# Optimization experiments

Measured on AMD Instinct MI355X. Metric: run time of the kernel, lower is better.

## Reference

```python
import jax, jax.numpy as jnp
import numpy as np

NEG_INF = -1e9
T = 0.07

def _l2norm(x, axis):
    return x / jnp.maximum(jnp.linalg.norm(x, axis=axis, keepdims=True), 1e-12)

def setup_inputs() -> dict:
    key = jax.random.key(0)
    ks = jax.random.split(key, 8)
    B, D, K, C = 1024, 128, 131072, 10
    q = jax.random.normal(ks[0], (B, D), dtype=jnp.float32)
    k = jax.random.normal(ks[1], (B, D), dtype=jnp.float32)
    labels = jax.random.randint(ks[2], (B,), 0, C)
    predictions = jax.random.randint(ks[3], (B,), 0, C)
    pos_queue = _l2norm(jax.random.normal(ks[4], (D, K), dtype=jnp.float32), axis=0)
    neg_queue = _l2norm(jax.random.normal(ks[5], (D, K), dtype=jnp.float32), axis=0)
    queue_labels = jax.random.randint(ks[6], (K,), 0, C)
    queue_predictions = jax.random.randint(ks[7], (K,), 0, C)
    return {"q": q, "k": k, "labels": labels, "predictions": predictions,
            "pos_queue": pos_queue, "neg_queue": neg_queue,
            "queue_labels": queue_labels, "queue_predictions": queue_predictions}

def _masked_mean_sim(qn, queue, sel_mask):
    # qn: [B,D], queue: [D,K], sel_mask: [B,K] bool
    sims = jnp.einsum('bd,dk->bk', qn, queue)            # [B,K]
    cnt = sel_mask.sum(axis=1)                           # [B]
    s = jnp.where(sel_mask, sims, 0.0).sum(axis=1)       # [B]
    return jnp.where(cnt > 0, s / jnp.maximum(cnt, 1).astype(sims.dtype), NEG_INF)

def reference(q, k, labels, predictions, pos_queue, neg_queue, queue_labels, queue_predictions):
    qn = _l2norm(q, axis=1)
    _ = _l2norm(k, axis=1)  # k normalized in original forward but unused downstream
    match = queue_predictions[None, :] == predictions[:, None]   # [B,K]
    correct = (queue_predictions == queue_labels)[None, :]       # [1,K]
    pos_mask = match & correct
    neg_mask = match & ~correct
    pos_logits = _masked_mean_sim(qn, pos_queue, pos_mask)       # [B]
    neg_logits = _masked_mean_sim(qn, neg_queue, neg_mask)       # [B]
    logits = jnp.stack([pos_logits, neg_logits], axis=1) / T     # [B,2]
    # cross entropy with target class 0, reduction='none'
    contrast_loss = -jax.nn.log_softmax(logits, axis=1)[:, 0]
    pred = jnp.argmax(logits, axis=1)
    acc = (pred == 0).astype(jnp.float32).mean()
    return contrast_loss, acc
```

## Files before the change

kernel.cpp:

```cpp
#include <hip/hip_runtime.h>

#define K_Q   131072
#define B_N   1024
#define D_DIM 128
#define NCLS  10
#define NC2   (2 * NCLS)
#define CHUNKS 16
#define NEG_INF_F (-1e9f)

__global__ void k_init(int* cnt, int* accCnt) {
    int t = threadIdx.x;
    if (t < NC2) cnt[t] = 0;
    if (t == 0) *accCnt = 0;
}

__global__ void k_code(const int* __restrict__ qp, const int* __restrict__ ql,
                       unsigned char* __restrict__ code, int* __restrict__ cnt) {
    __shared__ int lc[NC2];
    int t = threadIdx.x;
    if (t < NC2) lc[t] = 0;
    __syncthreads();
    int idx = blockIdx.x * blockDim.x + t;
    int stride = gridDim.x * blockDim.x;
    for (int k = idx; k < K_Q; k += stride) {
        int p = qp[k];
        int cd = (p == ql[k]) ? p : (p + NCLS);
        code[k] = (unsigned char)cd;
        atomicAdd(&lc[cd], 1);
    }
    __syncthreads();
    if (t < NC2) atomicAdd(&cnt[t], lc[t]);
}

__global__ __launch_bounds__(256, 4)
void k_reduce(const float* __restrict__ posq, const float* __restrict__ negq,
              const unsigned char* __restrict__ code,
              float* __restrict__ partial) {
    __shared__ float acc[256 * NC2];
    const int d  = blockIdx.y;
    const int ch = blockIdx.x;
    const int t  = threadIdx.x;
    const int span = K_Q / CHUNKS;
    const int k0 = ch * span;

    float* my = &acc[t * NC2];
#pragma unroll
    for (int j = 0; j < NC2; ++j) my[j] = 0.0f;
    __syncthreads();

    const float4* prow = (const float4*)(posq + (size_t)d * K_Q + k0);
    const float4* nrow = (const float4*)(negq + (size_t)d * K_Q + k0);
    const uchar4* crow = (const uchar4*)(code + k0);

    const int iters = span / 4 / 256;

    float4 pv = prow[t];
    float4 nv = nrow[t];
    uchar4 cd = crow[t];

    for (int it = 0; it < iters; ++it) {
        float4 cpv = pv, cnv = nv;
        uchar4 ccd = cd;
        int nx = (it + 1) * 256 + t;
        if (it + 1 < iters) {
            pv = prow[nx];
            nv = nrow[nx];
            cd = crow[nx];
        }
        {
            int c0 = ccd.x; my[c0] += (c0 < NCLS) ? cpv.x : cnv.x;
            int c1 = ccd.y; my[c1] += (c1 < NCLS) ? cpv.y : cnv.y;
            int c2 = ccd.z; my[c2] += (c2 < NCLS) ? cpv.z : cnv.z;
            int c3 = ccd.w; my[c3] += (c3 < NCLS) ? cpv.w : cnv.w;
        }
    }
    __syncthreads();

    if (t < 128) {
#pragma unroll
        for (int j = 0; j < NC2; ++j) acc[t * NC2 + j] += acc[(t + 128) * NC2 + j];
    }
    __syncthreads();
    if (t < 64) {
#pragma unroll
        for (int j = 0; j < NC2; ++j) acc[t * NC2 + j] += acc[(t + 64) * NC2 + j];
    }
    __syncthreads();

    if (t < 64) {
        float r[NC2];
#pragma unroll
        for (int j = 0; j < NC2; ++j) {
            float x = acc[t * NC2 + j];
#pragma unroll
            for (int off = 32; off; off >>= 1) x += __shfl_xor(x, off);
            r[j] = x;
        }
        if (t == 0) {
#pragma unroll
            for (int j = 0; j < NC2; ++j)
                partial[((size_t)d * CHUNKS + ch) * NC2 + j] = r[j];
        }
    }
}

__global__ void k_finalize(const float* __restrict__ partial, float* __restrict__ S) {
    int t = blockIdx.x * blockDim.x + threadIdx.x;
    if (t >= D_DIM * NC2) return;
    int d = t / NC2;
    int j = t % NC2;
    float s = 0.0f;
#pragma unroll
    for (int ch = 0; ch < CHUNKS; ++ch)
        s += partial[((size_t)d * CHUNKS + ch) * NC2 + j];
    S[j * D_DIM + d] = s;
}

__global__ void k_loss(const float* __restrict__ q, const int* __restrict__ preds,
                       const float* __restrict__ S, const int* __restrict__ cnt,
                       float* __restrict__ out, int* __restrict__ accCnt) {
    const int b = blockIdx.x;
    const int t = threadIdx.x;
    const int c = preds[b];

    float qv = q[(size_t)b * D_DIM + t];
    float sp = S[c * D_DIM + t];
    float sn = S[(NCLS + c) * D_DIM + t];
    float s0 = qv * qv, s1 = qv * sp, s2 = qv * sn;

#pragma unroll
    for (int off = 32; off; off >>= 1) {
        s0 += __shfl_xor(s0, off);
        s1 += __shfl_xor(s1, off);
        s2 += __shfl_xor(s2, off);
    }
    __shared__ float red[2][3];
    int wave = t >> 6;
    if ((t & 63) == 0) { red[wave][0] = s0; red[wave][1] = s1; red[wave][2] = s2; }
    __syncthreads();
    if (t == 0) {
        float nq  = red[0][0] + red[1][0];
        float dp  = red[0][1] + red[1][1];
        float dn  = red[0][2] + red[1][2];
        float inv = 1.0f / fmaxf(sqrtf(nq), 1e-12f);
        int cp = cnt[c], cn = cnt[NCLS + c];
        float pl = (cp > 0) ? (dp * inv) / (float)(cp > 1 ? cp : 1) : NEG_INF_F;
        float nl = (cn > 0) ? (dn * inv) / (float)(cn > 1 ? cn : 1) : NEG_INF_F;
        float a  = pl / 0.07f;
        float bb = nl / 0.07f;
        float m  = fmaxf(a, bb);
        float loss = m + logf(expf(a - m) + expf(bb - m)) - a;
        out[b] = loss;
        if (a >= bb) atomicAdd(accCnt, 1);
    }
}

__global__ void k_acc(const int* __restrict__ accCnt, float* __restrict__ out) {
    out[B_N] = (float)(*accCnt) * (1.0f / (float)B_N);
}

extern "C" void kernel_launch(void* const* d_in, const int* in_sizes, int n_in,
                              void* d_out, int out_size, void* d_ws, size_t ws_size,
                              hipStream_t stream) {
    const float* q      = (const float*)d_in[0];
    const int* preds    = (const int*)d_in[3];
    const float* posq   = (const float*)d_in[4];
    const float* negq   = (const float*)d_in[5];
    const int* qlabels  = (const int*)d_in[6];
    const int* qpreds   = (const int*)d_in[7];
    float* out = (float*)d_out;

    char* ws = (char*)d_ws;
    unsigned char* code = (unsigned char*)ws;
    int* cnt            = (int*)(ws + 131072);
    int* accCnt         = (int*)(ws + 131072 + 80);
    float* partial      = (float*)(ws + 131168);
    float* S            = (float*)(ws + 131168 + D_DIM * CHUNKS * NC2 * 4);

    k_init<<<1, 64, 0, stream>>>(cnt, accCnt);
    k_code<<<256, 256, 0, stream>>>(qpreds, qlabels, code, cnt);
    k_reduce<<<dim3(CHUNKS, D_DIM), 256, 0, stream>>>(posq, negq, code, partial);
    k_finalize<<<10, 256, 0, stream>>>(partial, S);
    k_loss<<<B_N, 128, 0, stream>>>(q, preds, S, cnt, out, accCnt);
    k_acc<<<1, 1, 0, stream>>>(accCnt, out);
}
```

Before: 47.62 us.

## Replace scalar class-bucketed reduction with bf16 MFMA one-hot matmul

The per-class sum over the queue is rewritten as a matrix product between one-hot class-indicator matrices and the queue rows, computed with bf16 16x16x32 MFMA instructions. Queue values are converted from fp32 to bf16 in registers, and each block covers a contiguous K slice across all D, writing per-block partials. A two-stage finalize then reduces those partials. This removes the LDS scatter-accumulate, but it adds bf16 rounding error and reads the K dimension through strided per-lane row accesses.

```diff
diff --git a/kernel.cpp b/kernel.cpp
--- a/kernel.cpp
+++ b/kernel.cpp
@@ -1,12 +1,25 @@
 #include <hip/hip_runtime.h>
+#include <hip/hip_bf16.h>
 
 #define K_Q   131072
 #define B_N   1024
 #define D_DIM 128
 #define NCLS  10
-#define NC2   (2 * NCLS)
-#define CHUNKS 16
+#define NC2   20
 #define NEG_INF_F (-1e9f)
+
+#define MBLK  512
+#define MW    4
+#define MSL   2
+#define FCH   8
+
+typedef __attribute__((ext_vector_type(8))) short short8v;
+typedef __attribute__((ext_vector_type(4))) float vf4;
+
+__device__ __forceinline__ short f2bf(float f) {
+    __hip_bfloat16 h = __float2bfloat16(f);
+    return *reinterpret_cast<short*>(&h);
+}
 
 __global__ void k_init(int* cnt, int* accCnt) {
     int t = threadIdx.x;
@@ -32,88 +45,100 @@
     if (t < NC2) atomicAdd(&cnt[t], lc[t]);
 }
 
-__global__ __launch_bounds__(256, 4)
-void k_reduce(const float* __restrict__ posq, const float* __restrict__ negq,
-              const unsigned char* __restrict__ code,
-              float* __restrict__ partial) {
-    __shared__ float acc[256 * NC2];
-    const int d  = blockIdx.y;
-    const int ch = blockIdx.x;
-    const int t  = threadIdx.x;
-    const int span = K_Q / CHUNKS;
-    const int k0 = ch * span;
-
-    float* my = &acc[t * NC2];
-#pragma unroll
-    for (int j = 0; j < NC2; ++j) my[j] = 0.0f;
-    __syncthreads();
-
-    const float4* prow = (const float4*)(posq + (size_t)d * K_Q + k0);
-    const float4* nrow = (const float4*)(negq + (size_t)d * K_Q + k0);
-    const uchar4* crow = (const uchar4*)(code + k0);
-
-    const int iters = span / 4 / 256;
-
-    float4 pv = prow[t];
-    float4 nv = nrow[t];
-    uchar4 cd = crow[t];
-
-    for (int it = 0; it < iters; ++it) {
-        float4 cpv = pv, cnv = nv;
-        uchar4 ccd = cd;
-        int nx = (it + 1) * 256 + t;
-        if (it + 1 < iters) {
-            pv = prow[nx];
-            nv = nrow[nx];
-            cd = crow[nx];
+__global__ __launch_bounds__(256)
+void k_mfma(const float* __restrict__ posq, const float* __restrict__ negq,
+            const unsigned char* __restrict__ code, float* __restrict__ partial) {
+    const int t    = threadIdx.x;
+    const int wave = t >> 6;
+    const int lane = t & 63;
+    const int bid  = blockIdx.x;
+    const int cl   = lane & 15;
+    const int g    = lane >> 4;
+
+    vf4 accp[8], accn[8];
+#pragma unroll
+    for (int i = 0; i < 8; ++i) {
+        accp[i] = (vf4){0.f, 0.f, 0.f, 0.f};
+        accn[i] = (vf4){0.f, 0.f, 0.f, 0.f};
+    }
+
+    for (int s = 0; s < MSL; ++s) {
+        const int gslice = (bid * MW + wave) * MSL + s;
+        const int kl = gslice * 32 + g * 8;
+
+        uint2 cw = *(const uint2*)(code + kl);
+        short8v ap, an;
+#pragma unroll
+        for (int j = 0; j < 8; ++j) {
+            unsigned b = (((j < 4) ? cw.x : cw.y) >> (8 * (j & 3))) & 0xffu;
+            ap[j] = (b == (unsigned)cl)          ? (short)0x3F80 : (short)0;
+            an[j] = (b == (unsigned)(cl + NCLS)) ? (short)0x3F80 : (short)0;
         }
-        {
-            int c0 = ccd.x; my[c0] += (c0 < NCLS) ? cpv.x : cnv.x;
-            int c1 = ccd.y; my[c1] += (c1 < NCLS) ? cpv.y : cnv.y;
-            int c2 = ccd.z; my[c2] += (c2 < NCLS) ? cpv.z : cnv.z;
-            int c3 = ccd.w; my[c3] += (c3 < NCLS) ? cpv.w : cnv.w;
+
+#pragma unroll
+        for (int db = 0; db < 8; ++db) {
+            const int d = db * 16 + cl;
+            const float* pp = posq + (size_t)d * K_Q + kl;
+            const float* np = negq + (size_t)d * K_Q + kl;
+            float4 p0 = ((const float4*)pp)[0];
+            float4 p1 = ((const float4*)pp)[1];
+            float4 n0 = ((const float4*)np)[0];
+            float4 n1 = ((const float4*)np)[1];
+            short8v bp, bn;
+            bp[0] = f2bf(p0.x); bp[1] = f2bf(p0.y); bp[2] = f2bf(p0.z); bp[3] = f2bf(p0.w);
+            bp[4] = f2bf(p1.x); bp[5] = f2bf(p1.y); bp[6] = f2bf(p1.z); bp[7] = f2bf(p1.w);
+            bn[0] = f2bf(n0.x); bn[1] = f2bf(n0.y); bn[2] = f2bf(n0.z); bn[3] = f2bf(n0.w);
+            bn[4] = f2bf(n1.x); bn[5] = f2bf(n1.y); bn[6] = f2bf(n1.z); bn[7] = f2bf(n1.w);
+            accp[db] = __builtin_amdgcn_mfma_f32_16x16x32_bf16(ap, bp, accp[db], 0, 0, 0);
+            accn[db] = __builtin_amdgcn_mfma_f32_16x16x32_bf16(an, bn, accn[db], 0, 0, 0);
         }
     }
-    __syncthreads();
-
-    if (t < 128) {
-#pragma unroll
-        for (int j = 0; j < NC2; ++j) acc[t * NC2 + j] += acc[(t + 128) * NC2 + j];
-    }
-    __syncthreads();
-    if (t < 64) {
-#pragma unroll
-        for (int j = 0; j < NC2; ++j) acc[t * NC2 + j] += acc[(t + 64) * NC2 + j];
-    }
-    __syncthreads();
-
-    if (t < 64) {
-        float r[NC2];
-#pragma unroll
-        for (int j = 0; j < NC2; ++j) {
-            float x = acc[t * NC2 + j];
-#pragma unroll
-            for (int off = 32; off; off >>= 1) x += __shfl_xor(x, off);
-            r[j] = x;
+
+    __shared__ float red[MW][64][8];
+#pragma unroll
+    for (int db = 0; db < 8; ++db) {
+        *(vf4*)&red[wave][lane][0] = accp[db];
+        *(vf4*)&red[wave][lane][4] = accn[db];
+        __syncthreads();
+        if (wave == 0) {
+#pragma unroll
+            for (int r = 0; r < 4; ++r) {
+                int cls = g * 4 + r;
+                if (cls < NCLS) {
+                    float sp = red[0][lane][r]     + red[1][lane][r]
+                             + red[2][lane][r]     + red[3][lane][r];
+                    float sn = red[0][lane][4 + r] + red[1][lane][4 + r]
+                             + red[2][lane][4 + r] + red[3][lane][4 + r];
+                    partial[((size_t)bid * NC2 + cls)        * D_DIM + db * 16 + cl] = sp;
+                    partial[((size_t)bid * NC2 + NCLS + cls) * D_DIM + db * 16 + cl] = sn;
+                }
+            }
         }
-        if (t == 0) {
-#pragma unroll
-            for (int j = 0; j < NC2; ++j)
-                partial[((size_t)d * CHUNKS + ch) * NC2 + j] = r[j];
-        }
-    }
-}
-
-__global__ void k_finalize(const float* __restrict__ partial, float* __restrict__ S) {
-    int t = blockIdx.x * blockDim.x + threadIdx.x;
-    if (t >= D_DIM * NC2) return;
-    int d = t / NC2;
-    int j = t % NC2;
+        __syncthreads();
+    }
+}
+
+__global__ void k_fin1(const float* __restrict__ partial, float* __restrict__ ws2) {
+    int idx = blockIdx.x * blockDim.x + threadIdx.x;
+    if (idx >= FCH * NC2 * D_DIM) return;
+    int chunk = idx / (NC2 * D_DIM);
+    int jd    = idx % (NC2 * D_DIM);
     float s = 0.0f;
-#pragma unroll
-    for (int ch = 0; ch < CHUNKS; ++ch)
-        s += partial[((size_t)d * CHUNKS + ch) * NC2 + j];
-    S[j * D_DIM + d] = s;
+    int b0 = chunk * (MBLK / FCH);
+#pragma unroll 8
+    for (int b = b0; b < b0 + MBLK / FCH; ++b)
+        s += partial[(size_t)b * (NC2 * D_DIM) + jd];
+    ws2[(size_t)chunk * (NC2 * D_DIM) + jd] = s;
+}
+
+__global__ void k_fin2(const float* __restrict__ ws2, float* __restrict__ S) {
+    int jd = blockIdx.x * blockDim.x + threadIdx.x;
+    if (jd >= NC2 * D_DIM) return;
+    float s = 0.0f;
+#pragma unroll
+    for (int ch = 0; ch < FCH; ++ch)
+        s += ws2[(size_t)ch * (NC2 * D_DIM) + jd];
+    S[jd] = s;
 }
 
 __global__ void k_loss(const float* __restrict__ q, const int* __restrict__ preds,
@@ -174,13 +199,15 @@
     unsigned char* code = (unsigned char*)ws;
     int* cnt            = (int*)(ws + 131072);
     int* accCnt         = (int*)(ws + 131072 + 80);
-    float* partial      = (float*)(ws + 131168);
-    float* S            = (float*)(ws + 131168 + D_DIM * CHUNKS * NC2 * 4);
+    float* partial      = (float*)(ws + 131328);
+    float* ws2          = (float*)(ws + 131328 + (size_t)MBLK * NC2 * D_DIM * 4);
+    float* S            = (float*)(ws + 131328 + (size_t)(MBLK + FCH) * NC2 * D_DIM * 4);
 
     k_init<<<1, 64, 0, stream>>>(cnt, accCnt);
     k_code<<<256, 256, 0, stream>>>(qpreds, qlabels, code, cnt);
-    k_reduce<<<dim3(CHUNKS, D_DIM), 256, 0, stream>>>(posq, negq, code, partial);
-    k_finalize<<<10, 256, 0, stream>>>(partial, S);
+    k_mfma<<<MBLK, 256, 0, stream>>>(posq, negq, code, partial);
+    k_fin1<<<(FCH * NC2 * D_DIM + 255) / 256, 256, 0, stream>>>(partial, ws2);
+    k_fin2<<<(NC2 * D_DIM + 255) / 256, 256, 0, stream>>>(ws2, S);
     k_loss<<<B_N, 128, 0, stream>>>(q, preds, S, cnt, out, accCnt);
     k_acc<<<1, 1, 0, stream>>>(accCnt, out);
 }
```

Measured after the change: 57.95 us. 21.7% more time.

## Fold partial-sum finalize and accuracy kernels into the loss kernel

Applied to the files above, without the earlier changes.

Reorders the partial buffer so each (class, d) row holds its chunk partials contiguously, then sums them inside the loss kernel with float4 loads, which removes the separate finalize kernel. The accuracy is now accumulated directly into the output with a float atomicAdd of 1/B, which removes the final single-thread kernel and the integer counter. This cuts two kernel launches in exchange for redundant partial summation in every loss block, and float atomic accumulation whose order can vary between runs.

```diff
diff --git a/kernel.cpp b/kernel.cpp
--- a/kernel.cpp
+++ b/kernel.cpp
@@ -4,14 +4,14 @@
 #define B_N   1024
 #define D_DIM 128
 #define NCLS  10
-#define NC2   (2 * NCLS)
+#define NC2   20
 #define CHUNKS 16
 #define NEG_INF_F (-1e9f)
 
-__global__ void k_init(int* cnt, int* accCnt) {
+__global__ void k_init(int* cnt, float* out) {
     int t = threadIdx.x;
     if (t < NC2) cnt[t] = 0;
-    if (t == 0) *accCnt = 0;
+    if (t == 0) out[B_N] = 0.0f;
 }
 
 __global__ void k_code(const int* __restrict__ qp, const int* __restrict__ ql,
@@ -99,35 +99,31 @@
         if (t == 0) {
 #pragma unroll
             for (int j = 0; j < NC2; ++j)
-                partial[((size_t)d * CHUNKS + ch) * NC2 + j] = r[j];
+                partial[((size_t)j * D_DIM + d) * CHUNKS + ch] = r[j];
         }
     }
 }
 
-__global__ void k_finalize(const float* __restrict__ partial, float* __restrict__ S) {
-    int t = blockIdx.x * blockDim.x + threadIdx.x;
-    if (t >= D_DIM * NC2) return;
-    int d = t / NC2;
-    int j = t % NC2;
-    float s = 0.0f;
-#pragma unroll
-    for (int ch = 0; ch < CHUNKS; ++ch)
-        s += partial[((size_t)d * CHUNKS + ch) * NC2 + j];
-    S[j * D_DIM + d] = s;
-}
-
 __global__ void k_loss(const float* __restrict__ q, const int* __restrict__ preds,
-                       const float* __restrict__ S, const int* __restrict__ cnt,
-                       float* __restrict__ out, int* __restrict__ accCnt) {
+                       const float* __restrict__ partial, const int* __restrict__ cnt,
+                       float* __restrict__ out) {
     const int b = blockIdx.x;
     const int t = threadIdx.x;
     const int c = preds[b];
 
     float qv = q[(size_t)b * D_DIM + t];
-    float sp = S[c * D_DIM + t];
-    float sn = S[(NCLS + c) * D_DIM + t];
+
+    const float4* pp = (const float4*)(partial + ((size_t)c * D_DIM + t) * CHUNKS);
+    const float4* pn = (const float4*)(partial + ((size_t)(c + NCLS) * D_DIM + t) * CHUNKS);
+    float sp = 0.f, sn = 0.f;
+#pragma unroll
+    for (int i = 0; i < 4; ++i) {
+        float4 a = pp[i], bq = pn[i];
+        sp += a.x + a.y + a.z + a.w;
+        sn += bq.x + bq.y + bq.z + bq.w;
+    }
+
     float s0 = qv * qv, s1 = qv * sp, s2 = qv * sn;
-
 #pragma unroll
     for (int off = 32; off; off >>= 1) {
         s0 += __shfl_xor(s0, off);
@@ -151,12 +147,8 @@
         float m  = fmaxf(a, bb);
         float loss = m + logf(expf(a - m) + expf(bb - m)) - a;
         out[b] = loss;
-        if (a >= bb) atomicAdd(accCnt, 1);
+        if (a >= bb) atomicAdd(&out[B_N], 1.0f / (float)B_N);
     }
-}
-
-__global__ void k_acc(const int* __restrict__ accCnt, float* __restrict__ out) {
-    out[B_N] = (float)(*accCnt) * (1.0f / (float)B_N);
 }
 
 extern "C" void kernel_launch(void* const* d_in, const int* in_sizes, int n_in,
@@ -173,14 +165,10 @@
     char* ws = (char*)d_ws;
     unsigned char* code = (unsigned char*)ws;
     int* cnt            = (int*)(ws + 131072);
-    int* accCnt         = (int*)(ws + 131072 + 80);
-    float* partial      = (float*)(ws + 131168);
-    float* S            = (float*)(ws + 131168 + D_DIM * CHUNKS * NC2 * 4);
+    float* partial      = (float*)(ws + 131328);
 
-    k_init<<<1, 64, 0, stream>>>(cnt, accCnt);
+    k_init<<<1, 64, 0, stream>>>(cnt, out);
     k_code<<<256, 256, 0, stream>>>(qpreds, qlabels, code, cnt);
     k_reduce<<<dim3(CHUNKS, D_DIM), 256, 0, stream>>>(posq, negq, code, partial);
-    k_finalize<<<10, 256, 0, stream>>>(partial, S);
-    k_loss<<<B_N, 128, 0, stream>>>(q, preds, S, cnt, out, accCnt);
-    k_acc<<<1, 1, 0, stream>>>(accCnt, out);
+    k_loss<<<B_N, 128, 0, stream>>>(q, preds, partial, cnt, out);
 }
```

New measurement: 46.35 us. 1.03x faster.
